# Performance work log

Hardware: AMD Instinct MI355X
Metric: run time of the kernel (lower is better)

## Reference

```python
import jax, jax.numpy as jnp
import numpy as np

ALPHA = 0.2  # LeakyReLU negative slope
NEG_BIG = -9e15

def setup_inputs() -> dict:
    key = jax.random.key(0)
    k1, k2, k3, k4, k5 = jax.random.split(key, 5)
    N, IN, OUT = 12288, 512, 256
    inp = jax.random.normal(k1, (N, IN), dtype=jnp.float32)
    adj = jax.random.randint(k2, (N, N), 0, 2, dtype=jnp.int32)
    # xavier_uniform with gain=1.414
    def xavier(k, shape, gain=1.414):
        fan_in, fan_out = shape[0], shape[1]
        bound = gain * np.sqrt(6.0 / (fan_in + fan_out))
        return jax.random.uniform(k, shape, dtype=jnp.float32, minval=-bound, maxval=bound)
    W = xavier(k3, (IN, OUT))
    a1 = xavier(k4, (OUT, 1))
    a2 = xavier(k5, (OUT, 1))
    return {"inp": inp, "adj": adj, "W": W, "a1": a1, "a2": a2}

def reference(inp, adj, W, a1, a2):
    h = inp @ W                      # [N, OUT]
    s1 = h @ a1                      # [N, 1]
    s2 = h @ a2                      # [N, 1]
    e = jax.nn.leaky_relu(s1 + s2.T, negative_slope=ALPHA)   # [N, N]
    scores = jnp.where(adj > 0, e, NEG_BIG)
    attention = jax.nn.softmax(scores, axis=1)               # row-wise softmax
    # dropout is identity in eval mode (training=False)
    h_prime = attention @ h          # [N, OUT]
    return jax.nn.elu(h_prime)       # concat=True -> elu
```

## Files before the change

kernel.cpp:

```cpp
#include <hip/hip_runtime.h>
#include <stdint.h>
#include <stddef.h>

#define NN     12288
#define INF    512
#define OUTF   256
#define ALPHA  0.2f
#define LOG2E  1.44269504088896340736f
#define PARTS  16
#define KRANGE (NN / PARTS)
#define NIT    (KRANGE / 64)

typedef __attribute__((ext_vector_type(4))) float          f32x4;
typedef __attribute__((ext_vector_type(8))) short          bf16x8;
typedef __attribute__((ext_vector_type(4))) unsigned int   u32x4;
typedef __attribute__((ext_vector_type(2))) unsigned int   u32x2;
typedef __attribute__((ext_vector_type(4))) unsigned short u16x4;

static __device__ __forceinline__ unsigned short f2bf(float f) {
  union { float f; unsigned u; } v; v.f = f;
  unsigned r = v.u + 0x7fffu + ((v.u >> 16) & 1u);
  return (unsigned short)(r >> 16);
}
static __device__ __forceinline__ float bf2f(unsigned short s) {
  union { unsigned u; float f; } v; v.u = ((unsigned)s) << 16;
  return v.f;
}


__global__ __launch_bounds__(256) void kc_bitmap(const int* __restrict__ adj,
                                                 unsigned char* __restrict__ bm) {
  const int t = threadIdx.x, l = t & 63, wv = t >> 6;
  const int gw = blockIdx.x * 4 + wv;
  const int* ip = adj + (size_t)gw * 18432 + l * 4;
  unsigned char* ob = bm + (size_t)gw * 2304 + (l >> 1);
  const bool writer = (l & 1) == 0;
  for (int i = 0; i < 72; i += 4) {
    u32x4 x[4];
#pragma unroll
    for (int u = 0; u < 4; ++u)
      x[u] = *(const u32x4*)(ip + (size_t)(i + u) * 256);
#pragma unroll
    for (int u = 0; u < 4; ++u) {
      const unsigned nib = min(x[u].x, 1u) | (min(x[u].y, 1u) << 1) |
                           (min(x[u].z, 1u) << 2) | (min(x[u].w, 1u) << 3);
      const unsigned other = (unsigned)__shfl_xor((int)nib, 1);
      if (writer) ob[(i + u) * 32] = (unsigned char)(nib | (other << 4));
    }
  }
}

__global__ __launch_bounds__(256) void k1_gemm_h(const float* __restrict__ inp,
                                                 const float* __restrict__ W,
                                                 const float* __restrict__ a1,
                                                 const float* __restrict__ a2,
                                                 unsigned short* __restrict__ hT,
                                                 float* __restrict__ s1,
                                                 float* __restrict__ s2) {
  __shared__ __align__(16) float inp_s[32][36];
  __shared__ __align__(16) float W_s[32][256];
  const int t = threadIdx.x;
  const int row0 = blockIdx.x * 32;
  const int tx = t & 63, ty = t >> 6;
  f32x4 acc[8];
#pragma unroll
  for (int r = 0; r < 8; ++r) acc[r] = f32x4{0.f, 0.f, 0.f, 0.f};
  for (int kc = 0; kc < 16; ++kc) {
    {
      const int r = t >> 3, ko = (t & 7) * 4;
      *(f32x4*)&inp_s[r][ko] = *(const f32x4*)(inp + (size_t)(row0 + r) * INF + kc * 32 + ko);
    }
#pragma unroll
    for (int j = 0; j < 8; ++j) {
      const int r = j * 4 + ty;
      *(f32x4*)&W_s[r][tx * 4] = *(const f32x4*)(W + (size_t)(kc * 32 + r) * OUTF + tx * 4);
    }
    __syncthreads();
#pragma unroll 4
    for (int k = 0; k < 32; ++k) {
      const f32x4 wv = *(const f32x4*)&W_s[k][tx * 4];
#pragma unroll
      for (int rr = 0; rr < 8; ++rr) acc[rr] += inp_s[ty * 8 + rr][k] * wv;
    }
    __syncthreads();
  }
#pragma unroll
  for (int rr = 0; rr < 8; ++rr) *(f32x4*)&W_s[ty * 8 + rr][tx * 4] = acc[rr];
  __syncthreads();
  {
    const int col = t;
    char* dst = (char*)hT + (size_t)col * (NN * 2) + (size_t)(row0 >> 6) * 128;
    const unsigned swz = (unsigned)((col & 7) << 4);
    const unsigned wbase = (unsigned)(row0 & 63) * 2;
#pragma unroll
    for (int s = 0; s < 4; ++s) {
      unsigned e0 = (unsigned)f2bf(W_s[s*8+0][col]) | ((unsigned)f2bf(W_s[s*8+1][col]) << 16);
      unsigned e1 = (unsigned)f2bf(W_s[s*8+2][col]) | ((unsigned)f2bf(W_s[s*8+3][col]) << 16);
      unsigned e2 = (unsigned)f2bf(W_s[s*8+4][col]) | ((unsigned)f2bf(W_s[s*8+5][col]) << 16);
      unsigned e3 = (unsigned)f2bf(W_s[s*8+6][col]) | ((unsigned)f2bf(W_s[s*8+7][col]) << 16);
      u32x4 p; p.x = e0; p.y = e1; p.z = e2; p.w = e3;
      *(u32x4*)(dst + ((wbase + (unsigned)s * 16) ^ swz)) = p;
    }
  }
  {
    const int r = t >> 3, seg = t & 7;
    const float* hrow = &W_s[r][seg * 32];
    float v1 = 0.f, v2 = 0.f;
#pragma unroll
    for (int dd = 0; dd < 32; dd += 4) {
      const f32x4 hv  = *(const f32x4*)(hrow + dd);
      const f32x4 a1v = *(const f32x4*)(a1 + seg * 32 + dd);
      const f32x4 a2v = *(const f32x4*)(a2 + seg * 32 + dd);
      v1 += hv.x*a1v.x + hv.y*a1v.y + hv.z*a1v.z + hv.w*a1v.w;
      v2 += hv.x*a2v.x + hv.y*a2v.y + hv.z*a2v.z + hv.w*a2v.w;
    }
    v1 += __shfl_xor(v1, 1); v1 += __shfl_xor(v1, 2); v1 += __shfl_xor(v1, 4);
    v2 += __shfl_xor(v2, 1); v2 += __shfl_xor(v2, 2); v2 += __shfl_xor(v2, 4);
    if (seg == 0) { s1[row0 + r] = v1; s2[row0 + r] = v2; }
  }
}

__global__ __launch_bounds__(1024) void k3_s2max(const float* __restrict__ s2,
                                                 float* __restrict__ s2max) {
  __shared__ float red[1024];
  const int t = threadIdx.x;
  float m = -3.0e38f;
  for (int j = t; j < NN; j += 1024) m = fmaxf(m, s2[j]);
  red[t] = m;
  __syncthreads();
  for (int s = 512; s > 0; s >>= 1) {
    if (t < s) red[t] = fmaxf(red[t], red[t + s]);
    __syncthreads();
  }
  if (t == 0) s2max[0] = red[0];
}


#define GLDS16(SRC, DST)                                                        \
  __builtin_amdgcn_global_load_lds(                                             \
      (const __attribute__((address_space(1))) unsigned int*)(SRC),             \
      (__attribute__((address_space(3))) unsigned int*)(DST), 16, 0, 0)

#define K4_STAGE(BUF, IT)                                                       \
  do {                                                                          \
    const size_t _coff = (size_t)(kword0 + (IT)) * 128;                         \
    _Pragma("unroll") for (int _p = 0; _p < 8; ++_p) {                          \
      const int _idx = _p * 256 + t;                                            \
      const char* _src = (const char*)hT + (size_t)(_idx >> 3) * (NN * 2) +     \
                         _coff + (size_t)(_idx & 7) * 16;                       \
      GLDS16(_src, (char*)B_lds + (size_t)(BUF) * 32768 +                       \
                       (size_t)(_p * 256 + (wv << 6)) * 16);                    \
    }                                                                           \
  } while (0)

#define K4_PREFETCH(DST, IT)                                                    \
  do {                                                                          \
    DST[0] = *(const u32x2*)(bmr0 + (IT) * 8);                                  \
    DST[1] = *(const u32x2*)(bmr1 + (IT) * 8);                                  \
  } while (0)

#define K4_COMPUTE(BMC, IT)                                                     \
  do {                                                                          \
    _Pragma("unroll") for (int _kt = 0; _kt < 2; ++_kt) {                       \
      const f32x4 _sa = *(const f32x4*)(s2_lds + (IT) * 64 + _kt * 32 + ko * 8);\
      const f32x4 _sb = *(const f32x4*)(s2_lds + (IT) * 64 + _kt * 32 + ko * 8 + 4);\
      _Pragma("unroll") for (int _rt = 0; _rt < 2; ++_rt) {                     \
        const unsigned _w32 = (_kt == 0) ? BMC[_rt].x : BMC[_rt].y;             \
        const unsigned _byte = (_w32 >> ko8) & 0xFFu;                           \
        bf16x8 _f;                                                              \
        _Pragma("unroll") for (int _j = 0; _j < 4; ++_j) {                      \
          const float _tt = s1v[_rt] + _sa[_j];                                 \
          const float _e = fmaxf(_tt, ALPHA * _tt);                             \
          float _w = 0.f;                                                       \
          if (_byte & (1u << _j))                                               \
            _w = exp2f(__builtin_fmaf(_e, LOG2E, -ML2[_rt]));                   \
          dsum[_rt] += _w;                                                      \
          _f[_j] = (short)f2bf(_w);                                            \
        }                                                                       \
        _Pragma("unroll") for (int _j = 0; _j < 4; ++_j) {                      \
          const float _tt = s1v[_rt] + _sb[_j];                                 \
          const float _e = fmaxf(_tt, ALPHA * _tt);                             \
          float _w = 0.f;                                                       \
          if (_byte & (16u << _j))                                              \
            _w = exp2f(__builtin_fmaf(_e, LOG2E, -ML2[_rt]));                   \
          dsum[_rt] += _w;                                                      \
          _f[4 + _j] = (short)f2bf(_w);                                        \
        }                                                                       \
        frag[_rt][_kt] = _f;                                                    \
      }                                                                         \
    }                                                                           \
  } while (0)

#define K4_MFMA(BUF)                                                            \
  do {                                                                          \
    const char* _Bb = (const char*)B_lds + (size_t)(BUF) * 32768;               \
    _Pragma("unroll") for (int _kt = 0; _kt < 2; ++_kt) {                       \
      const unsigned _kb = (unsigned)((_kt * 32 + ko * 8) * 2);                 \
      _Pragma("unroll") for (int _ct = 0; _ct < 16; ++_ct) {                    \
        const int _col = _ct * 16 + m;                                          \
        const bf16x8 _b = *(const bf16x8*)(_Bb + _col * 128 +                   \
                              (_kb ^ ((unsigned)((_col & 7) << 4))));           \
        acc[0][_ct] = __builtin_amdgcn_mfma_f32_16x16x32_bf16(frag[0][_kt], _b, \
                                                              acc[0][_ct], 0, 0, 0);\
        acc[1][_ct] = __builtin_amdgcn_mfma_f32_16x16x32_bf16(frag[1][_kt], _b, \
                                                              acc[1][_ct], 0, 0, 0);\
      }                                                                         \
    }                                                                           \
  } while (0)

#define K4_BARRIER()                                                            \
  do {                                                                          \
    asm volatile("s_waitcnt vmcnt(2)" ::: "memory");                            \
    __builtin_amdgcn_sched_barrier(0);                                          \
    __builtin_amdgcn_s_barrier();                                               \
    __builtin_amdgcn_sched_barrier(0);                                          \
  } while (0)

#define K4_SUB(IT, BUF, BCUR, BNXT, ISLAST)                                     \
  do {                                                                          \
    if (!(ISLAST)) {                                                            \
      K4_STAGE((BUF) ^ 1, (IT) + 1);                                            \
      __builtin_amdgcn_sched_barrier(0);                                        \
    }                                                                           \
    K4_COMPUTE(BCUR, IT);                                                       \
    if (!(ISLAST)) K4_PREFETCH(BNXT, (IT) + 1);                                 \
    K4_MFMA(BUF);                                                               \
    if (!(ISLAST)) K4_BARRIER();                                                \
  } while (0)

__global__ __launch_bounds__(256, 2) void k4_attn(const unsigned char* __restrict__ bm,
                                                  const unsigned short* __restrict__ hT,
                                                  const float* __restrict__ s1,
                                                  const float* __restrict__ s2,
                                                  const float* __restrict__ s2max,
                                                  unsigned short* __restrict__ accp,
                                                  float* __restrict__ denp) {
  __shared__ __align__(16) char B_lds[2][256 * 128];
  __shared__ __align__(16) float s2_lds[KRANGE];
  const int t = threadIdx.x;
  const int wv = t >> 6, l = t & 63;
  const int m = l & 15, ko = l >> 4;
  const int ko8 = ko * 8;
  const int wgid = (blockIdx.x % 8) * 192 + blockIdx.x / 8;
  const int part = wgid / 96, rb = wgid % 96;
  const int row0 = rb * 128 + wv * 32;
  const int kbase = part * KRANGE;
  const int kword0 = kbase >> 6;

  const float S2MAX = s2max[0];
  float s1v[2], ML2[2], dsum[2];
#pragma unroll
  for (int rt = 0; rt < 2; ++rt) {
    s1v[rt] = s1[row0 + rt * 16 + m];
    const float tup = s1v[rt] + S2MAX;
    const float M = fmaxf(tup, ALPHA * tup);
    ML2[rt] = M * LOG2E;
    dsum[rt] = 0.f;
  }
  f32x4 acc[2][16];
#pragma unroll
  for (int rt = 0; rt < 2; ++rt)
#pragma unroll
    for (int ct = 0; ct < 16; ++ct) acc[rt][ct] = f32x4{0.f, 0.f, 0.f, 0.f};

  const unsigned char* bmr0 = bm + (size_t)(row0 + m) * (NN / 8) + (kbase >> 3);
  const unsigned char* bmr1 = bmr0 + (size_t)16 * (NN / 8);
  u32x2 bmE[2], bmO[2];
  bf16x8 frag[2][2];

  {
    if (wv < 3)
      GLDS16((const char*)(s2 + kbase) + (size_t)t * 16, (char*)s2_lds + ((size_t)wv << 10));
    K4_STAGE(0, 0);
    __builtin_amdgcn_sched_barrier(0);
    K4_PREFETCH(bmE, 0);
    K4_BARRIER();
  }

#pragma unroll 1
  for (int it = 0; it < NIT - 2; it += 2) {
    K4_SUB(it, 0, bmE, bmO, false);
    K4_SUB(it + 1, 1, bmO, bmE, false);
  }
  K4_SUB(NIT - 2, 0, bmE, bmO, false);
  K4_SUB(NIT - 1, 1, bmO, bmE, true);

#pragma unroll
  for (int rt = 0; rt < 2; ++rt) {
    dsum[rt] += __shfl_xor(dsum[rt], 16);
    dsum[rt] += __shfl_xor(dsum[rt], 32);
  }
  if (l < 16) {
    denp[(size_t)part * NN + row0 + l] = dsum[0];
    denp[(size_t)part * NN + row0 + 16 + l] = dsum[1];
  }
  unsigned short* ap = accp + (size_t)part * NN * OUTF;
#pragma unroll
  for (int rt = 0; rt < 2; ++rt)
#pragma unroll
    for (int ct = 0; ct < 16; ++ct) {
      const int col = ct * 16 + m;
      const int grow = row0 + rt * 16 + ko * 4;
#pragma unroll
      for (int j = 0; j < 4; ++j)
        ap[(size_t)(grow + j) * OUTF + col] = f2bf(acc[rt][ct][j]);
    }
}

__global__ __launch_bounds__(256) void k5_combine(const unsigned short* __restrict__ accp,
                                                  const float* __restrict__ denp,
                                                  float* __restrict__ out) {
  const int idx = blockIdx.x * 256 + threadIdx.x;
  const int row = idx >> 6;
  f32x4 v = f32x4{0.f, 0.f, 0.f, 0.f};
  float den = 0.f;
#pragma unroll
  for (int p = 0; p < PARTS; ++p) {
    const u16x4 pv = *(const u16x4*)(accp + (size_t)p * NN * OUTF + (size_t)idx * 4);
    v.x += bf2f(pv.x); v.y += bf2f(pv.y); v.z += bf2f(pv.z); v.w += bf2f(pv.w);
    den += denp[(size_t)p * NN + row];
  }
  const float inv = 1.f / den;
  f32x4 r;
#pragma unroll
  for (int j = 0; j < 4; ++j) {
    const float x = v[j] * inv;
    r[j] = x > 0.f ? x : (__expf(x) - 1.f);
  }
  *(f32x4*)(out + (size_t)idx * 4) = r;
}

extern "C" void kernel_launch(void* const* d_in, const int* in_sizes, int n_in,
                              void* d_out, int out_size, void* d_ws, size_t ws_size,
                              hipStream_t stream) {
  const float* inp = (const float*)d_in[0];
  const int*   adj = (const int*)d_in[1];
  const float* W   = (const float*)d_in[2];
  const float* a1  = (const float*)d_in[3];
  const float* a2  = (const float*)d_in[4];
  float* out = (float*)d_out;
  char* ws = (char*)d_ws;

  unsigned short* hT  = (unsigned short*)(ws + 0);
  float* s1   = (float*)(ws + 6291456);
  float* s2   = (float*)(ws + 6340608);
  float* s2m  = (float*)(ws + 6389760);
  unsigned char* bmp = (unsigned char*)(ws + 6390016);
  unsigned short* accp = (unsigned short*)(ws + 25264384);
  float* denp = (float*)(ws + 125927680);

  kc_bitmap<<<dim3(2048), dim3(256), 0, stream>>>(adj, bmp);
  k1_gemm_h<<<dim3(NN / 32), dim3(256), 0, stream>>>(inp, W, a1, a2, hT, s1, s2);
  k3_s2max<<<dim3(1), dim3(1024), 0, stream>>>(s2, s2m);
  k4_attn<<<dim3(96 * PARTS), dim3(256), 0, stream>>>(bmp, hT, s1, s2, s2m, accp, denp);
  k5_combine<<<dim3(NN * OUTF / 1024), dim3(256), 0, stream>>>(accp, denp, out);
}
```

Before: 421.2 us.

## Interleave LDS reads, staging and MFMA in attention loop; fuse bitmap with h GEMM

The attention kernel's main loop is split into four sub-blocks per iteration. Each sub-block loads its B fragments from LDS into registers, issues half of the next tile's global-to-LDS staging, computes one slice of the exp weights, then runs a block of MFMAs at raised priority with barriers between sub-blocks. This aims to overlap LDS, global and VALU work with matrix math across waves. Separately, the adjacency-bitmap and h-GEMM kernels are merged into one launch by dispatching on block index. The cost is extra barriers per iteration and more register pressure from the held B fragments.

```diff
diff --git a/kernel.cpp b/kernel.cpp
--- a/kernel.cpp
+++ b/kernel.cpp
@@ -28,39 +28,45 @@
 }
 
 
-__global__ __launch_bounds__(256) void kc_bitmap(const int* __restrict__ adj,
-                                                 unsigned char* __restrict__ bm) {
-  const int t = threadIdx.x, l = t & 63, wv = t >> 6;
-  const int gw = blockIdx.x * 4 + wv;
-  const int* ip = adj + (size_t)gw * 18432 + l * 4;
-  unsigned char* ob = bm + (size_t)gw * 2304 + (l >> 1);
-  const bool writer = (l & 1) == 0;
-  for (int i = 0; i < 72; i += 4) {
-    u32x4 x[4];
-#pragma unroll
-    for (int u = 0; u < 4; ++u)
-      x[u] = *(const u32x4*)(ip + (size_t)(i + u) * 256);
-#pragma unroll
-    for (int u = 0; u < 4; ++u) {
-      const unsigned nib = min(x[u].x, 1u) | (min(x[u].y, 1u) << 1) |
-                           (min(x[u].z, 1u) << 2) | (min(x[u].w, 1u) << 3);
-      const unsigned other = (unsigned)__shfl_xor((int)nib, 1);
-      if (writer) ob[(i + u) * 32] = (unsigned char)(nib | (other << 4));
-    }
-  }
-}
-
-__global__ __launch_bounds__(256) void k1_gemm_h(const float* __restrict__ inp,
-                                                 const float* __restrict__ W,
-                                                 const float* __restrict__ a1,
-                                                 const float* __restrict__ a2,
-                                                 unsigned short* __restrict__ hT,
-                                                 float* __restrict__ s1,
-                                                 float* __restrict__ s2) {
+#define KC_BLOCKS 2048
+#define K1_BLOCKS 384
+
+__global__ __launch_bounds__(256) void ka_fused(const float* __restrict__ inp,
+                                                const int* __restrict__ adj,
+                                                const float* __restrict__ W,
+                                                const float* __restrict__ a1,
+                                                const float* __restrict__ a2,
+                                                unsigned short* __restrict__ hT,
+                                                float* __restrict__ s1,
+                                                float* __restrict__ s2,
+                                                unsigned char* __restrict__ bm) {
   __shared__ __align__(16) float inp_s[32][36];
   __shared__ __align__(16) float W_s[32][256];
   const int t = threadIdx.x;
-  const int row0 = blockIdx.x * 32;
+
+  if (blockIdx.x < KC_BLOCKS) {
+    const int l = t & 63, wv = t >> 6;
+    const int gw = blockIdx.x * 4 + wv;
+    const int* ip = adj + (size_t)gw * 18432 + l * 4;
+    unsigned char* ob = bm + (size_t)gw * 2304 + (l >> 1);
+    const bool writer = (l & 1) == 0;
+    for (int i = 0; i < 72; i += 4) {
+      u32x4 x[4];
+#pragma unroll
+      for (int u = 0; u < 4; ++u)
+        x[u] = *(const u32x4*)(ip + (size_t)(i + u) * 256);
+#pragma unroll
+      for (int u = 0; u < 4; ++u) {
+        const unsigned nib = min(x[u].x, 1u) | (min(x[u].y, 1u) << 1) |
+                             (min(x[u].z, 1u) << 2) | (min(x[u].w, 1u) << 3);
+        const unsigned other = (unsigned)__shfl_xor((int)nib, 1);
+        if (writer) ob[(i + u) * 32] = (unsigned char)(nib | (other << 4));
+      }
+    }
+    return;
+  }
+
+  const int row0 = (blockIdx.x - KC_BLOCKS) * 32;
   const int tx = t & 63, ty = t >> 6;
   f32x4 acc[8];
 #pragma unroll
@@ -78,9 +84,9 @@
     __syncthreads();
 #pragma unroll 4
     for (int k = 0; k < 32; ++k) {
-      const f32x4 wv = *(const f32x4*)&W_s[k][tx * 4];
-#pragma unroll
-      for (int rr = 0; rr < 8; ++rr) acc[rr] += inp_s[ty * 8 + rr][k] * wv;
+      const f32x4 wv2 = *(const f32x4*)&W_s[k][tx * 4];
+#pragma unroll
+      for (int rr = 0; rr < 8; ++rr) acc[rr] += inp_s[ty * 8 + rr][k] * wv2;
     }
     __syncthreads();
   }
@@ -141,10 +147,12 @@
       (const __attribute__((address_space(1))) unsigned int*)(SRC),             \
       (__attribute__((address_space(3))) unsigned int*)(DST), 16, 0, 0)
 
-#define K4_STAGE(BUF, IT)                                                       \
+#define SGB0 __builtin_amdgcn_sched_barrier(0)
+
+#define K4_STAGE4(BUF, IT, HALF)                                                \
   do {                                                                          \
     const size_t _coff = (size_t)(kword0 + (IT)) * 128;                         \
-    _Pragma("unroll") for (int _p = 0; _p < 8; ++_p) {                          \
+    _Pragma("unroll") for (int _p = (HALF) * 4; _p < (HALF) * 4 + 4; ++_p) {    \
       const int _idx = _p * 256 + t;                                            \
       const char* _src = (const char*)hT + (size_t)(_idx >> 3) * (NN * 2) +     \
                          _coff + (size_t)(_idx & 7) * 16;                       \
@@ -159,73 +167,94 @@
     DST[1] = *(const u32x2*)(bmr1 + (IT) * 8);                                  \
   } while (0)
 
-#define K4_COMPUTE(BMC, IT)                                                     \
-  do {                                                                          \
-    _Pragma("unroll") for (int _kt = 0; _kt < 2; ++_kt) {                       \
-      const f32x4 _sa = *(const f32x4*)(s2_lds + (IT) * 64 + _kt * 32 + ko * 8);\
-      const f32x4 _sb = *(const f32x4*)(s2_lds + (IT) * 64 + _kt * 32 + ko * 8 + 4);\
-      _Pragma("unroll") for (int _rt = 0; _rt < 2; ++_rt) {                     \
-        const unsigned _w32 = (_kt == 0) ? BMC[_rt].x : BMC[_rt].y;             \
-        const unsigned _byte = (_w32 >> ko8) & 0xFFu;                           \
-        bf16x8 _f;                                                              \
-        _Pragma("unroll") for (int _j = 0; _j < 4; ++_j) {                      \
-          const float _tt = s1v[_rt] + _sa[_j];                                 \
-          const float _e = fmaxf(_tt, ALPHA * _tt);                             \
-          float _w = 0.f;                                                       \
-          if (_byte & (1u << _j))                                               \
-            _w = exp2f(__builtin_fmaf(_e, LOG2E, -ML2[_rt]));                   \
-          dsum[_rt] += _w;                                                      \
-          _f[_j] = (short)f2bf(_w);                                            \
-        }                                                                       \
-        _Pragma("unroll") for (int _j = 0; _j < 4; ++_j) {                      \
-          const float _tt = s1v[_rt] + _sb[_j];                                 \
-          const float _e = fmaxf(_tt, ALPHA * _tt);                             \
-          float _w = 0.f;                                                       \
-          if (_byte & (16u << _j))                                              \
-            _w = exp2f(__builtin_fmaf(_e, LOG2E, -ML2[_rt]));                   \
-          dsum[_rt] += _w;                                                      \
-          _f[4 + _j] = (short)f2bf(_w);                                        \
-        }                                                                       \
-        frag[_rt][_kt] = _f;                                                    \
+#define K4_CSLICE(BMC, IT, KT)                                                  \
+  do {                                                                          \
+    const f32x4 _sa = *(const f32x4*)(s2_lds + (IT) * 64 + (KT) * 32 + ko * 8); \
+    const f32x4 _sb = *(const f32x4*)(s2_lds + (IT) * 64 + (KT) * 32 + ko * 8 + 4); \
+    _Pragma("unroll") for (int _rt = 0; _rt < 2; ++_rt) {                       \
+      const unsigned _w32 = ((KT) == 0) ? BMC[_rt].x : BMC[_rt].y;              \
+      const unsigned _byte = (_w32 >> ko8) & 0xFFu;                             \
+      bf16x8 _f;                                                                \
+      _Pragma("unroll") for (int _j = 0; _j < 4; ++_j) {                        \
+        const float _tt = s1v[_rt] + _sa[_j];                                   \
+        const float _e = fmaxf(_tt, ALPHA * _tt);                               \
+        float _w = 0.f;                                                         \
+        if (_byte & (1u << _j))                                                 \
+          _w = exp2f(__builtin_fmaf(_e, LOG2E, -ML2[_rt]));                     \
+        dsum[_rt] += _w;                                                        \
+        _f[_j] = (short)f2bf(_w);                                               \
       }                                                                         \
-    }                                                                           \
-  } while (0)
-
-#define K4_MFMA(BUF)                                                            \
+      _Pragma("unroll") for (int _j = 0; _j < 4; ++_j) {                        \
+        const float _tt = s1v[_rt] + _sb[_j];                                   \
+        const float _e = fmaxf(_tt, ALPHA * _tt);                               \
+        float _w = 0.f;                                                         \
+        if (_byte & (16u << _j))                                                \
+          _w = exp2f(__builtin_fmaf(_e, LOG2E, -ML2[_rt]));                     \
+        dsum[_rt] += _w;                                                        \
+        _f[4 + _j] = (short)f2bf(_w);                                           \
+      }                                                                         \
+      frag[_rt][KT] = _f;                                                       \
+    }                                                                           \
+  } while (0)
+
+#define K4_DS8(BUF, G, BR)                                                      \
   do {                                                                          \
     const char* _Bb = (const char*)B_lds + (size_t)(BUF) * 32768;               \
-    _Pragma("unroll") for (int _kt = 0; _kt < 2; ++_kt) {                       \
-      const unsigned _kb = (unsigned)((_kt * 32 + ko * 8) * 2);                 \
-      _Pragma("unroll") for (int _ct = 0; _ct < 16; ++_ct) {                    \
-        const int _col = _ct * 16 + m;                                          \
-        const bf16x8 _b = *(const bf16x8*)(_Bb + _col * 128 +                   \
-                              (_kb ^ ((unsigned)((_col & 7) << 4))));           \
-        acc[0][_ct] = __builtin_amdgcn_mfma_f32_16x16x32_bf16(frag[0][_kt], _b, \
-                                                              acc[0][_ct], 0, 0, 0);\
-        acc[1][_ct] = __builtin_amdgcn_mfma_f32_16x16x32_bf16(frag[1][_kt], _b, \
-                                                              acc[1][_ct], 0, 0, 0);\
-      }                                                                         \
-    }                                                                           \
-  } while (0)
-
-#define K4_BARRIER()                                                            \
-  do {                                                                          \
-    asm volatile("s_waitcnt vmcnt(2)" ::: "memory");                            \
-    __builtin_amdgcn_sched_barrier(0);                                          \
+    const unsigned _kb = (unsigned)((((G) >> 1) * 32 + ko * 8) * 2);            \
+    _Pragma("unroll") for (int _c = 0; _c < 8; ++_c) {                          \
+      const int _col = (((G) & 1) * 8 + _c) * 16 + m;                           \
+      BR[_c] = *(const bf16x8*)(_Bb + _col * 128 +                              \
+                                (_kb ^ ((unsigned)((_col & 7) << 4))));         \
+    }                                                                           \
+  } while (0)
+
+#define K4_MFMABLK(G, BR)                                                       \
+  do {                                                                          \
+    SGB0;                                                                       \
     __builtin_amdgcn_s_barrier();                                               \
-    __builtin_amdgcn_sched_barrier(0);                                          \
-  } while (0)
-
-#define K4_SUB(IT, BUF, BCUR, BNXT, ISLAST)                                     \
-  do {                                                                          \
-    if (!(ISLAST)) {                                                            \
-      K4_STAGE((BUF) ^ 1, (IT) + 1);                                            \
-      __builtin_amdgcn_sched_barrier(0);                                        \
-    }                                                                           \
-    K4_COMPUTE(BCUR, IT);                                                       \
-    if (!(ISLAST)) K4_PREFETCH(BNXT, (IT) + 1);                                 \
-    K4_MFMA(BUF);                                                               \
-    if (!(ISLAST)) K4_BARRIER();                                                \
+    asm volatile("s_waitcnt lgkmcnt(0)" ::: "memory");                          \
+    SGB0;                                                                       \
+    __builtin_amdgcn_s_setprio(1);                                              \
+    _Pragma("unroll") for (int _c = 0; _c < 8; ++_c) {                          \
+      const int _ct = ((G) & 1) * 8 + _c;                                       \
+      acc[0][_ct] = __builtin_amdgcn_mfma_f32_16x16x32_bf16(frag[0][(G) >> 1],  \
+                        BR[_c], acc[0][_ct], 0, 0, 0);                          \
+      acc[1][_ct] = __builtin_amdgcn_mfma_f32_16x16x32_bf16(frag[1][(G) >> 1],  \
+                        BR[_c], acc[1][_ct], 0, 0, 0);                          \
+    }                                                                           \
+    __builtin_amdgcn_s_setprio(0);                                              \
+    SGB0;                                                                       \
+  } while (0)
+
+#define K4_ITER(IT, BUF, BMC, BMN, LAST)                                        \
+  do {                                                                          \
+    bf16x8 br[8];                                                               \
+                                 \
+    K4_DS8(BUF, 0, br);                                                         \
+    if (!(LAST)) K4_STAGE4((BUF) ^ 1, (IT) + 1, 0);                             \
+    K4_CSLICE(BMC, IT, 0);                                                      \
+    K4_MFMABLK(0, br);                                                          \
+    __builtin_amdgcn_s_barrier();                                               \
+                                 \
+    K4_DS8(BUF, 1, br);                                                         \
+    if (!(LAST)) K4_STAGE4((BUF) ^ 1, (IT) + 1, 1);                             \
+    K4_CSLICE(BMC, IT, 1);                                                      \
+    K4_MFMABLK(1, br);                                                          \
+    __builtin_amdgcn_s_barrier();                                               \
+                                      \
+    K4_DS8(BUF, 2, br);                                                         \
+    if (!(LAST)) K4_PREFETCH(BMN, (IT) + 1);                                    \
+    K4_MFMABLK(2, br);                                                          \
+    __builtin_amdgcn_s_barrier();                                               \
+                                 \
+    K4_DS8(BUF, 3, br);                                                         \
+    K4_MFMABLK(3, br);                                                          \
+    if (!(LAST)) {                                                              \
+      asm volatile("s_waitcnt vmcnt(2)" ::: "memory");                          \
+      SGB0;                                                                     \
+      __builtin_amdgcn_s_barrier();                                             \
+      SGB0;                                                                     \
+    }                                                                           \
   } while (0)
 
 __global__ __launch_bounds__(256, 2) void k4_attn(const unsigned char* __restrict__ bm,
@@ -271,19 +300,21 @@
   {
     if (wv < 3)
       GLDS16((const char*)(s2 + kbase) + (size_t)t * 16, (char*)s2_lds + ((size_t)wv << 10));
-    K4_STAGE(0, 0);
-    __builtin_amdgcn_sched_barrier(0);
+    K4_STAGE4(0, 0, 0);
+    K4_STAGE4(0, 0, 1);
+    SGB0;
     K4_PREFETCH(bmE, 0);
-    K4_BARRIER();
+    asm volatile("s_waitcnt vmcnt(2)" ::: "memory");
+    SGB0;
+    __builtin_amdgcn_s_barrier();
+    SGB0;
   }
 
 #pragma unroll 1
-  for (int it = 0; it < NIT - 2; it += 2) {
-    K4_SUB(it, 0, bmE, bmO, false);
-    K4_SUB(it + 1, 1, bmO, bmE, false);
-  }
-  K4_SUB(NIT - 2, 0, bmE, bmO, false);
-  K4_SUB(NIT - 1, 1, bmO, bmE, true);
+  for (int it = 0; it < NIT; it += 2) {
+    K4_ITER(it, 0, bmE, bmO, false);
+    K4_ITER(it + 1, 1, bmO, bmE, (it + 2 >= NIT));
+  }
 
 #pragma unroll
   for (int rt = 0; rt < 2; ++rt) {
@@ -349,8 +380,8 @@
   unsigned short* accp = (unsigned short*)(ws + 25264384);
   float* denp = (float*)(ws + 125927680);
 
-  kc_bitmap<<<dim3(2048), dim3(256), 0, stream>>>(adj, bmp);
-  k1_gemm_h<<<dim3(NN / 32), dim3(256), 0, stream>>>(inp, W, a1, a2, hT, s1, s2);
+  ka_fused<<<dim3(KC_BLOCKS + K1_BLOCKS), dim3(256), 0, stream>>>(inp, adj, W, a1, a2,
+                                                                  hT, s1, s2, bmp);
   k3_s2max<<<dim3(1), dim3(1024), 0, stream>>>(s2, s2m);
   k4_attn<<<dim3(96 * PARTS), dim3(256), 0, stream>>>(bmp, hT, s1, s2, s2m, accp, denp);
   k5_combine<<<dim3(NN * OUTF / 1024), dim3(256), 0, stream>>>(accp, denp, out);
```

New measurement: 485.3 us. 1.15x slower.

## Halve split-K parts, store fp32 partials nontemporally, widen bitmap packing per lane

Applied to the files above, without the earlier changes.

Cuts the number of split-K partitions in the attention kernel from 16 to 8, which doubles the per-block K range and halves the partial-sum traffic that the combine kernel reads. Partial accumulators are now stored as fp32 with nontemporal stores and loads instead of being rounded to bf16, removing the conversion and improving accuracy. The bitmap kernel now has each lane pack 8 adjacency entries into a byte directly, which removes the shuffle and the half-idle writer lanes. With half as many blocks, the attention kernel may have less parallelism to fill the GPU, and each fp32 partial costs twice the bytes.

```diff
diff --git a/kernel.cpp b/kernel.cpp
--- a/kernel.cpp
+++ b/kernel.cpp
@@ -7,7 +7,7 @@
 #define OUTF   256
 #define ALPHA  0.2f
 #define LOG2E  1.44269504088896340736f
-#define PARTS  16
+#define PARTS  8
 #define KRANGE (NN / PARTS)
 #define NIT    (KRANGE / 64)
 
@@ -15,38 +15,28 @@
 typedef __attribute__((ext_vector_type(8))) short          bf16x8;
 typedef __attribute__((ext_vector_type(4))) unsigned int   u32x4;
 typedef __attribute__((ext_vector_type(2))) unsigned int   u32x2;
-typedef __attribute__((ext_vector_type(4))) unsigned short u16x4;
 
 static __device__ __forceinline__ unsigned short f2bf(float f) {
   union { float f; unsigned u; } v; v.f = f;
   unsigned r = v.u + 0x7fffu + ((v.u >> 16) & 1u);
   return (unsigned short)(r >> 16);
 }
-static __device__ __forceinline__ float bf2f(unsigned short s) {
-  union { unsigned u; float f; } v; v.u = ((unsigned)s) << 16;
-  return v.f;
-}
 
 
 __global__ __launch_bounds__(256) void kc_bitmap(const int* __restrict__ adj,
                                                  unsigned char* __restrict__ bm) {
   const int t = threadIdx.x, l = t & 63, wv = t >> 6;
   const int gw = blockIdx.x * 4 + wv;
-  const int* ip = adj + (size_t)gw * 18432 + l * 4;
-  unsigned char* ob = bm + (size_t)gw * 2304 + (l >> 1);
-  const bool writer = (l & 1) == 0;
-  for (int i = 0; i < 72; i += 4) {
-    u32x4 x[4];
-#pragma unroll
-    for (int u = 0; u < 4; ++u)
-      x[u] = *(const u32x4*)(ip + (size_t)(i + u) * 256);
-#pragma unroll
-    for (int u = 0; u < 4; ++u) {
-      const unsigned nib = min(x[u].x, 1u) | (min(x[u].y, 1u) << 1) |
-                           (min(x[u].z, 1u) << 2) | (min(x[u].w, 1u) << 3);
-      const unsigned other = (unsigned)__shfl_xor((int)nib, 1);
-      if (writer) ob[(i + u) * 32] = (unsigned char)(nib | (other << 4));
-    }
+  const int* ip = adj + (size_t)gw * 18432 + l * 8;
+  unsigned char* ob = bm + (size_t)gw * 2304 + l;
+#pragma unroll 4
+  for (int i = 0; i < 36; ++i) {
+    const u32x4 x0 = *(const u32x4*)(ip + (size_t)i * 512);
+    const u32x4 x1 = *(const u32x4*)(ip + (size_t)i * 512 + 4);
+    unsigned b = min(x0.x, 1u) | (min(x0.y, 1u) << 1) | (min(x0.z, 1u) << 2) |
+                 (min(x0.w, 1u) << 3) | (min(x1.x, 1u) << 4) | (min(x1.y, 1u) << 5) |
+                 (min(x1.z, 1u) << 6) | (min(x1.w, 1u) << 7);
+    ob[i * 64] = (unsigned char)b;
   }
 }
 
@@ -78,9 +68,9 @@
     __syncthreads();
 #pragma unroll 4
     for (int k = 0; k < 32; ++k) {
-      const f32x4 wv = *(const f32x4*)&W_s[k][tx * 4];
-#pragma unroll
-      for (int rr = 0; rr < 8; ++rr) acc[rr] += inp_s[ty * 8 + rr][k] * wv;
+      const f32x4 wv2 = *(const f32x4*)&W_s[k][tx * 4];
+#pragma unroll
+      for (int rr = 0; rr < 8; ++rr) acc[rr] += inp_s[ty * 8 + rr][k] * wv2;
     }
     __syncthreads();
   }
@@ -162,8 +152,8 @@
 #define K4_COMPUTE(BMC, IT)                                                     \
   do {                                                                          \
     _Pragma("unroll") for (int _kt = 0; _kt < 2; ++_kt) {                       \
-      const f32x4 _sa = *(const f32x4*)(s2_lds + (IT) * 64 + _kt * 32 + ko * 8);\
-      const f32x4 _sb = *(const f32x4*)(s2_lds + (IT) * 64 + _kt * 32 + ko * 8 + 4);\
+      const f32x4 _sa = *(const f32x4*)(s2_lds + (IT) * 64 + _kt * 32 + ko8);   \
+      const f32x4 _sb = *(const f32x4*)(s2_lds + (IT) * 64 + _kt * 32 + ko8 + 4);\
       _Pragma("unroll") for (int _rt = 0; _rt < 2; ++_rt) {                     \
         const unsigned _w32 = (_kt == 0) ? BMC[_rt].x : BMC[_rt].y;             \
         const unsigned _byte = (_w32 >> ko8) & 0xFFu;                           \
@@ -195,7 +185,7 @@
   do {                                                                          \
     const char* _Bb = (const char*)B_lds + (size_t)(BUF) * 32768;               \
     _Pragma("unroll") for (int _kt = 0; _kt < 2; ++_kt) {                       \
-      const unsigned _kb = (unsigned)((_kt * 32 + ko * 8) * 2);                 \
+      const unsigned _kb = (unsigned)((_kt * 32 + ko8) * 2);                    \
       _Pragma("unroll") for (int _ct = 0; _ct < 16; ++_ct) {                    \
         const int _col = _ct * 16 + m;                                          \
         const bf16x8 _b = *(const bf16x8*)(_Bb + _col * 128 +                   \
@@ -233,7 +223,7 @@
                                                   const float* __restrict__ s1,
                                                   const float* __restrict__ s2,
                                                   const float* __restrict__ s2max,
-                                                  unsigned short* __restrict__ accp,
+                                                  float* __restrict__ accp,
                                                   float* __restrict__ denp) {
   __shared__ __align__(16) char B_lds[2][256 * 128];
   __shared__ __align__(16) float s2_lds[KRANGE];
@@ -241,7 +231,7 @@
   const int wv = t >> 6, l = t & 63;
   const int m = l & 15, ko = l >> 4;
   const int ko8 = ko * 8;
-  const int wgid = (blockIdx.x % 8) * 192 + blockIdx.x / 8;
+  const int wgid = (blockIdx.x % 8) * 96 + blockIdx.x / 8;
   const int part = wgid / 96, rb = wgid % 96;
   const int row0 = rb * 128 + wv * 32;
   const int kbase = part * KRANGE;
@@ -269,8 +259,11 @@
   bf16x8 frag[2][2];
 
   {
-    if (wv < 3)
-      GLDS16((const char*)(s2 + kbase) + (size_t)t * 16, (char*)s2_lds + ((size_t)wv << 10));
+    GLDS16((const char*)(s2 + kbase) + (size_t)t * 16,
+           (char*)s2_lds + (size_t)(wv << 6) * 16);
+    if (t < 128)
+      GLDS16((const char*)(s2 + kbase) + (size_t)(256 + t) * 16,
+             (char*)s2_lds + (size_t)(256 + (wv << 6)) * 16);
     K4_STAGE(0, 0);
     __builtin_amdgcn_sched_barrier(0);
     K4_PREFETCH(bmE, 0);
@@ -294,7 +287,7 @@
     denp[(size_t)part * NN + row0 + l] = dsum[0];
     denp[(size_t)part * NN + row0 + 16 + l] = dsum[1];
   }
-  unsigned short* ap = accp + (size_t)part * NN * OUTF;
+  float* ap = accp + (size_t)part * NN * OUTF;
 #pragma unroll
   for (int rt = 0; rt < 2; ++rt)
 #pragma unroll
@@ -303,11 +296,11 @@
       const int grow = row0 + rt * 16 + ko * 4;
 #pragma unroll
       for (int j = 0; j < 4; ++j)
-        ap[(size_t)(grow + j) * OUTF + col] = f2bf(acc[rt][ct][j]);
-    }
-}
-
-__global__ __launch_bounds__(256) void k5_combine(const unsigned short* __restrict__ accp,
+        __builtin_nontemporal_store(acc[rt][ct][j], &ap[(size_t)(grow + j) * OUTF + col]);
+    }
+}
+
+__global__ __launch_bounds__(256) void k5_combine(const float* __restrict__ accp,
                                                   const float* __restrict__ denp,
                                                   float* __restrict__ out) {
   const int idx = blockIdx.x * 256 + threadIdx.x;
@@ -316,8 +309,8 @@
   float den = 0.f;
 #pragma unroll
   for (int p = 0; p < PARTS; ++p) {
-    const u16x4 pv = *(const u16x4*)(accp + (size_t)p * NN * OUTF + (size_t)idx * 4);
-    v.x += bf2f(pv.x); v.y += bf2f(pv.y); v.z += bf2f(pv.z); v.w += bf2f(pv.w);
+    v += __builtin_nontemporal_load((const f32x4*)(accp + (size_t)p * NN * OUTF +
+                                                   (size_t)idx * 4));
     den += denp[(size_t)p * NN + row];
   }
   const float inv = 1.f / den;
@@ -346,7 +339,7 @@
   float* s2   = (float*)(ws + 6340608);
   float* s2m  = (float*)(ws + 6389760);
   unsigned char* bmp = (unsigned char*)(ws + 6390016);
-  unsigned short* accp = (unsigned short*)(ws + 25264384);
+  float* accp = (float*)(ws + 25264384);
   float* denp = (float*)(ws + 125927680);
 
   kc_bitmap<<<dim3(2048), dim3(256), 0, stream>>>(adj, bmp);
```

Result: slower. 447.0 us (+6.1%).
